# Optimization experiments

Hardware: AMD Instinct MI355X
Metric: run time of the kernel (lower is better)

## Reference

```python
import jax, jax.numpy as jnp
import numpy as np

B, T, P, H, D = 2, 2048, 1024, 16, 128
C = H * D  # 2048
ROPE_THETA = 10000.0


def setup_inputs() -> dict:
    key = jax.random.key(0)
    ks = jax.random.split(key, 5)
    x = jax.random.normal(ks[0], (B, T, C), jnp.float32)
    w_qkv = jax.random.normal(ks[1], (C, 3 * C), jnp.float32) * 0.02  # Linear(dim, 3*dim), applied as x @ w
    w_out = jax.random.normal(ks[2], (C, C), jnp.float32) * 0.02
    past_k = jax.random.normal(ks[3], (B, H, P, D), jnp.float32)
    past_v = jax.random.normal(ks[4], (B, H, P, D), jnp.float32)
    return {"x": x, "w_qkv": w_qkv, "w_out": w_out, "past_k": past_k, "past_v": past_v}


def _rope(q, k, offset):
    # rotate-half RoPE (GPT-NeoX style), positions offset..offset+T-1
    d = q.shape[-1]
    inv_freq = 1.0 / (ROPE_THETA ** (jnp.arange(0, d, 2, dtype=jnp.float32) / d))  # [d/2]
    pos = offset + jnp.arange(q.shape[2], dtype=jnp.float32)                        # [T]
    ang = pos[:, None] * inv_freq[None, :]                                          # [T, d/2]
    cos = jnp.concatenate([jnp.cos(ang), jnp.cos(ang)], -1)[None, None]             # [1,1,T,d]
    sin = jnp.concatenate([jnp.sin(ang), jnp.sin(ang)], -1)[None, None]

    def rot_half(t):
        t1, t2 = jnp.split(t, 2, axis=-1)
        return jnp.concatenate([-t2, t1], -1)

    return q * cos + rot_half(q) * sin, k * cos + rot_half(k) * sin


def reference(x, w_qkv, w_out, past_k, past_v):
    Bv, Tv, Cv = x.shape
    Hn = past_k.shape[1]
    Dd = Cv // Hn
    # fused QKV projection
    qkv = x @ w_qkv                       # [B,T,3C]
    q, k, v = jnp.split(qkv, 3, axis=-1)  # each [B,T,C]

    def split_heads(t):
        return t.reshape(Bv, Tv, Hn, Dd).transpose(0, 2, 1, 3)  # [B,H,T,D]

    q, k, v = split_heads(q), split_heads(k), split_heads(v)
    # RoPE with offset = past length
    q, k = _rope(q, k, past_k.shape[2])
    # KV-cache concat along time axis
    k = jnp.concatenate([past_k, k], axis=2)  # [B,H,P+T,D]
    v = jnp.concatenate([past_v, v], axis=2)
    # SDPA: past_kv present -> is_causal=False, no mask (full attention)
    scale = 1.0 / jnp.sqrt(jnp.float32(Dd))
    scores = jnp.einsum('bhqd,bhkd->bhqk', q, k) * scale
    attn = jax.nn.softmax(scores, axis=-1)
    out = jnp.einsum('bhqk,bhkd->bhqd', attn, v)
    out = out.transpose(0, 2, 1, 3).reshape(Bv, Tv, Cv)
    return out @ w_out
```

## Files before the change

### kernel.cpp

```cpp
#include <hip/hip_runtime.h>
#include <stdint.h>

#define B_ 2
#define T_ 2048
#define P_ 1024
#define H_ 16
#define D_ 128
#define C_ 2048
#define S_ 3072
#define M_ 4096
#define N3_ 6144

typedef unsigned short u16;
typedef unsigned int uint32;
typedef __attribute__((ext_vector_type(8))) short short8;
typedef __attribute__((ext_vector_type(8))) __bf16 bf16x8;
typedef __attribute__((ext_vector_type(4))) float f32x4;
typedef __attribute__((ext_vector_type(16))) float f32x16;
typedef __attribute__((ext_vector_type(4))) unsigned short u16x4;
typedef __attribute__((ext_vector_type(4))) unsigned int uint4v;

static __device__ __forceinline__ float bf2f(u16 h) {
    union { unsigned int u; float f; } x; x.u = ((unsigned int)h) << 16; return x.f;
}
static __device__ __forceinline__ u16 f2bf(float f) {
    return __builtin_bit_cast(u16, (__bf16)f);
}
static __device__ __forceinline__ uint32 cvtpk(float lo, float hi) {
    uint32 r;
    asm("v_cvt_pk_bf16_f32 %0, %1, %2" : "=v"(r) : "v"(lo), "v"(hi));
    return r;
}
#define MAX3(a, b, c) fmaxf(fmaxf((a), (b)), (c))

static __device__ __forceinline__ f32x16 mfma32(short8 a, short8 b, f32x16 c) {
    return __builtin_amdgcn_mfma_f32_32x32x16_bf16(
        __builtin_bit_cast(bf16x8, a), __builtin_bit_cast(bf16x8, b), c, 0, 0, 0);
}

typedef __attribute__((address_space(3))) unsigned int lds_u32;
typedef const __attribute__((address_space(1))) unsigned int glb_u32;
static __device__ __forceinline__ void gload_lds16(const void* g, void* l) {
    __builtin_amdgcn_global_load_lds((glb_u32*)g, (lds_u32*)l, 16, 0, 0);
}

static __device__ __forceinline__ void storeC(float* p, float v) { *p = v; }
static __device__ __forceinline__ void storeC(u16* p, float v) { *p = f2bf(v); }


__global__ void castx_kernel(const float* __restrict__ x, u16* __restrict__ Xb) {
    int idx = blockIdx.x * 256 + threadIdx.x;
    const float4 v = ((const float4*)x)[idx];
    u16x4 o;
    o.x = f2bf(v.x); o.y = f2bf(v.y); o.z = f2bf(v.z); o.w = f2bf(v.w);
    ((u16x4*)Xb)[idx] = o;
}

__global__ void wT_kernel(const float* __restrict__ W, u16* __restrict__ Wt,
                          int Ndim, int Kdim) {
    __shared__ float tile[64][65];
    const int n0 = blockIdx.x * 64, k0 = blockIdx.y * 64;
    const int tid = threadIdx.x;
#pragma unroll
    for (int i = 0; i < 16; i++) {
        int idx = tid + i * 256;
        int r = idx >> 6, c = idx & 63;
        tile[r][c] = W[(size_t)(k0 + r) * Ndim + n0 + c];
    }
    __syncthreads();
#pragma unroll
    for (int i = 0; i < 16; i++) {
        int idx = tid + i * 256;
        int r = idx >> 6, c = idx & 63;
        Wt[(size_t)(n0 + r) * Kdim + k0 + c] = f2bf(tile[c][r]);
    }
}

__global__ void rope_table_kernel(float* __restrict__ cosT, float* __restrict__ sinT) {
    int idx = blockIdx.x * 256 + threadIdx.x;
    int t = idx >> 6, d = idx & 63;
    float inv = powf(10000.0f, -(float)d * (1.0f / 64.0f));
    float ang = (float)(P_ + t) * inv;
    cosT[idx] = cosf(ang);
    sinT[idx] = sinf(ang);
}

__global__ void rope_qk_kernel(u16* __restrict__ QKVb, u16* __restrict__ Kc,
                               const float* __restrict__ cosT,
                               const float* __restrict__ sinT) {
    int idx = blockIdx.x * 256 + threadIdx.x;
    int d = idx & 63;
    int h = (idx >> 6) & 15;
    int t = (idx >> 10) & 2047;
    int b = idx >> 21;
    size_t rowoff = (size_t)(b * T_ + t) * N3_;
    float c = cosT[(t << 6) + d], s = sinT[(t << 6) + d];
    {
        u16* p1 = QKVb + rowoff + h * 128 + d;
        float x1 = bf2f(p1[0]), x2 = bf2f(p1[64]);
        p1[0]  = f2bf(x1 * c - x2 * s);
        p1[64] = f2bf(x2 * c + x1 * s);
    }
    {
        const u16* p1 = QKVb + rowoff + C_ + h * 128 + d;
        float x1 = bf2f(p1[0]), x2 = bf2f(p1[64]);
        u16* o = Kc + ((size_t)(b * H_ + h) * S_ + P_ + t) * 128 + d;
        o[0]  = f2bf(x1 * c - x2 * s);
        o[64] = f2bf(x2 * c + x1 * s);
    }
}

__global__ void pastk_kernel(const float* __restrict__ past_k, u16* __restrict__ Kc) {
    int idx = blockIdx.x * 256 + threadIdx.x;
    int d = idx & 127;
    int p = (idx >> 7) & 1023;
    int bh = idx >> 17;
    Kc[((size_t)bh * S_ + p) * 128 + d] = f2bf(past_k[idx]);
}

__global__ void vnewT_kernel(const u16* __restrict__ QKVb, u16* __restrict__ Vt) {
    __shared__ u16 tile[64][65];
    const int t0 = blockIdx.x * 64, d0 = blockIdx.y * 64, bh = blockIdx.z;
    const int b = bh >> 4, h = bh & 15;
    const int tid = threadIdx.x;
#pragma unroll
    for (int i = 0; i < 16; i++) {
        int idx = tid + i * 256;
        int r = idx >> 6, c = idx & 63;
        tile[r][c] = QKVb[(size_t)(b * T_ + t0 + r) * N3_ + 2 * C_ + h * 128 + d0 + c];
    }
    __syncthreads();
#pragma unroll
    for (int i = 0; i < 16; i++) {
        int idx = tid + i * 256;
        int r = idx >> 6, c = idx & 63;
        Vt[((size_t)bh * 128 + d0 + r) * S_ + P_ + t0 + c] = tile[c][r];
    }
}

__global__ void vpastT_kernel(const float* __restrict__ past_v, u16* __restrict__ Vt) {
    __shared__ float tile[64][65];
    const int p0 = blockIdx.x * 64, d0 = blockIdx.y * 64, bh = blockIdx.z;
    const int tid = threadIdx.x;
#pragma unroll
    for (int i = 0; i < 16; i++) {
        int idx = tid + i * 256;
        int r = idx >> 6, c = idx & 63;
        tile[r][c] = past_v[((size_t)bh * P_ + p0 + r) * 128 + d0 + c];
    }
    __syncthreads();
#pragma unroll
    for (int i = 0; i < 16; i++) {
        int idx = tid + i * 256;
        int r = idx >> 6, c = idx & 63;
        Vt[((size_t)bh * 128 + d0 + r) * S_ + p0 + c] = f2bf(tile[c][r]);
    }
}

template <typename OutT>
__global__ void __launch_bounds__(512, 1)
gemm3(const u16* __restrict__ A, const u16* __restrict__ Bt,
      OutT* __restrict__ Co, int Mdim, int Ndim, int Kdim) {
    __shared__ u16 lA[3 * 256 * 64];
    __shared__ u16 lB[3 * 128 * 64];
    const int nbx = Ndim >> 7;
    const int nwg = (Mdim >> 8) * nbx;
    int bid = blockIdx.x;
    int wg = (bid & 7) * (nwg >> 3) + (bid >> 3);
    const int bm = wg / nbx, bn = wg % nbx;
    const int m0 = bm << 8, n0 = bn << 7;
    const int tid = threadIdx.x;
    const int wave = tid >> 6, lane = tid & 63;
    const int mw = wave >> 1, nw = wave & 1;
    const int l31 = lane & 31, hi = lane >> 5;

    f32x16 acc[2][2];
#pragma unroll
    for (int i = 0; i < 2; i++)
#pragma unroll
        for (int j = 0; j < 2; j++) acc[i][j] = (f32x16)(0.0f);

    const u16* aSrc[4];
    const u16* bSrc[2];
#pragma unroll
    for (int i = 0; i < 4; i++) {
        int cid = i * 512 + tid;
        int r = cid >> 3, pc = cid & 7;
        aSrc[i] = A + (size_t)(m0 + r) * Kdim + ((pc ^ (r & 7)) << 3);
    }
#pragma unroll
    for (int i = 0; i < 2; i++) {
        int cid = i * 512 + tid;
        int r = cid >> 3, pc = cid & 7;
        bSrc[i] = Bt + (size_t)(n0 + r) * Kdim + ((pc ^ (r & 7)) << 3);
    }

#define STAGE3(bi, kt) do {                                                     \
    u16* _pa = lA + (bi) * 16384 + wave * 512;                                  \
    u16* _pb = lB + (bi) * 8192 + wave * 512;                                   \
    _Pragma("unroll")                                                           \
    for (int i = 0; i < 4; i++)                                                 \
        gload_lds16(aSrc[i] + (size_t)(kt) * 64, _pa + i * 4096);               \
    _Pragma("unroll")                                                           \
    for (int i = 0; i < 2; i++)                                                 \
        gload_lds16(bSrc[i] + (size_t)(kt) * 64, _pb + i * 4096);               \
} while (0)

    STAGE3(0, 0);
    STAGE3(1, 1);

    const int NT = Kdim >> 6;
    int bc = 0;
    for (int t = 0; t < NT; ++t) {
        if (t + 1 < NT) asm volatile("s_waitcnt vmcnt(6)" ::: "memory");
        else            asm volatile("s_waitcnt vmcnt(0)" ::: "memory");
        __builtin_amdgcn_s_barrier();
        asm volatile("" ::: "memory");
        if (t + 2 < NT) {
            int b2 = bc + 2; if (b2 >= 3) b2 -= 3;
            STAGE3(b2, t + 2);
        }
        const u16* la = lA + bc * 16384;
        const u16* lb = lB + bc * 8192;
        short8 af[2][4], bf[2][4];
#pragma unroll
        for (int mi = 0; mi < 2; mi++)
#pragma unroll
            for (int ks = 0; ks < 4; ks++) {
                int r = mw * 64 + mi * 32 + l31;
                int cb = ((ks << 5) + (hi << 4)) ^ ((r & 7) << 4);
                af[mi][ks] = *(const short8*)&la[r * 64 + (cb >> 1)];
            }
#pragma unroll
        for (int nj = 0; nj < 2; nj++)
#pragma unroll
            for (int ks = 0; ks < 4; ks++) {
                int r = nw * 64 + nj * 32 + l31;
                int cb = ((ks << 5) + (hi << 4)) ^ ((r & 7) << 4);
                bf[nj][ks] = *(const short8*)&lb[r * 64 + (cb >> 1)];
            }
        __builtin_amdgcn_s_setprio(1);
#pragma unroll
        for (int ks = 0; ks < 4; ks++)
#pragma unroll
            for (int mi = 0; mi < 2; mi++)
#pragma unroll
                for (int nj = 0; nj < 2; nj++)
                    acc[mi][nj] = mfma32(af[mi][ks], bf[nj][ks], acc[mi][nj]);
        __builtin_amdgcn_s_setprio(0);
        __builtin_amdgcn_sched_barrier(0);
        bc = bc + 1; if (bc >= 3) bc = 0;
    }
#undef STAGE3

#pragma unroll
    for (int mi = 0; mi < 2; mi++)
#pragma unroll
        for (int nj = 0; nj < 2; nj++) {
            int col = n0 + nw * 64 + nj * 32 + l31;
#pragma unroll
            for (int g = 0; g < 4; g++) {
                int row = m0 + mw * 64 + mi * 32 + g * 8 + hi * 4;
#pragma unroll
                for (int q = 0; q < 4; q++)
                    storeC(&Co[(size_t)(row + q) * Ndim + col],
                           acc[mi][nj][g * 4 + q]);
            }
        }
}

__global__ void __launch_bounds__(256, 2)
attn_kernel(const u16* __restrict__ QKVb, const u16* __restrict__ Kc,
            const u16* __restrict__ Vt, u16* __restrict__ O) {
    __shared__ u16 ldsK[2][64 * 128];
    __shared__ u16 ldsV[2][128 * 64];

    int bid = blockIdx.x;
    int wg = (bid & 7) * 64 + (bid >> 3);
    const int qc = wg & 15;
    const int bh = wg >> 4;
    const int b = bh >> 4, h = bh & 15;
    const int tid = threadIdx.x, wave = tid >> 6, lane = tid & 63;
    const int l31 = lane & 31, hi = lane >> 5;

    const int krow = tid >> 4;
    const int kcol = (((tid & 15) << 4) ^ ((krow & 7) << 4)) >> 1;
    const int vrow = tid >> 3;
    const int vcol = (((tid & 7) << 4) ^ ((vrow & 7) << 4)) >> 1;

    const u16* Kbh = Kc + (size_t)bh * S_ * 128;
    const u16* Vbh = Vt + (size_t)bh * 128 * S_;

    const int tq = qc * 128 + wave * 32 + l31;
    short8 qf[8];
    {
        const u16* qp = QKVb + (size_t)(b * T_ + tq) * N3_ + h * 128 + hi * 8;
#pragma unroll
        for (int ks = 0; ks < 8; ks++) qf[ks] = *(const short8*)(qp + ks * 16);
    }

    f32x16 acco[4];
#pragma unroll
    for (int d = 0; d < 4; d++) acco[d] = (f32x16)(0.0f);
    float mrow = -1e30f, lrow = 0.f;
    const float sl2 = 0.08838834764831845f * 1.4426950408889634f;

#define STAGE(bufi, tt) do {                                                    \
    const int _s0 = (tt) * 64;                                                  \
    _Pragma("unroll")                                                           \
    for (int i = 0; i < 4; i++)                                                 \
        gload_lds16(Kbh + (size_t)(_s0 + krow + i * 16) * 128 + kcol,           \
                    (char*)&ldsK[bufi][0] + i * 4096 + wave * 1024);            \
    _Pragma("unroll")                                                           \
    for (int i = 0; i < 4; i++)                                                 \
        gload_lds16(Vbh + (size_t)(vrow + i * 32) * S_ + _s0 + vcol,            \
                    (char*)&ldsV[bufi][0] + i * 4096 + wave * 1024);            \
} while (0)

    STAGE(0, 0);
    __syncthreads();

    const int swz = (l31 & 7) << 4;

    for (int t = 0; t < S_ / 64; ++t) {
        const int cur = t & 1;
        if (t < S_ / 64 - 1) STAGE(cur ^ 1, t + 1);

        const u16* Kl = ldsK[cur];
        const u16* Vl = ldsV[cur];

        f32x16 p0 = (f32x16)(0.0f), p1 = (f32x16)(0.0f);
        __builtin_amdgcn_s_setprio(1);
#pragma unroll
        for (int ks = 0; ks < 8; ks++) {
            const int cidx = (((ks * 32 + hi * 16) ^ swz) >> 1);
            short8 k0 = *(const short8*)&Kl[(l31 << 7) + cidx];
            short8 k1 = *(const short8*)&Kl[((32 + l31) << 7) + cidx];
            p0 = mfma32(k0, qf[ks], p0);
            p1 = mfma32(k1, qf[ks], p1);
        }
        __builtin_amdgcn_s_setprio(0);

        float t0 = MAX3(p0[0], p0[1], p0[2]);
        float t1 = MAX3(p0[3], p0[4], p0[5]);
        float t2 = MAX3(p0[6], p0[7], p0[8]);
        float t3 = MAX3(p0[9], p0[10], p0[11]);
        float t4 = MAX3(p0[12], p0[13], p0[14]);
        float t5 = MAX3(p0[15], p1[0], p1[1]);
        float t6 = MAX3(p1[2], p1[3], p1[4]);
        float t7 = MAX3(p1[5], p1[6], p1[7]);
        float t8 = MAX3(p1[8], p1[9], p1[10]);
        float t9 = MAX3(p1[11], p1[12], p1[13]);
        float u0 = MAX3(t0, t1, t2);
        float u1 = MAX3(t3, t4, t5);
        float u2 = MAX3(t6, t7, t8);
        float u3 = MAX3(t9, p1[14], p1[15]);
        float pm = fmaxf(MAX3(u0, u1, u2), u3);
        pm = fmaxf(pm, __shfl_xor(pm, 32));
        float pmS = pm * sl2;
        if (!__all(pmS <= mrow + 8.0f)) {
            float mn = fmaxf(mrow, pmS);
            float fac = exp2f(mrow - mn);
            mrow = mn;
            lrow *= fac;
#pragma unroll
            for (int d = 0; d < 4; d++)
#pragma unroll
                for (int r = 0; r < 16; r++) acco[d][r] *= fac;
        }
        float s0 = 0.f, s1 = 0.f, s2 = 0.f, s3 = 0.f;
#pragma unroll
        for (int r = 0; r < 16; r += 4) {
            p0[r + 0] = exp2f(fmaf(p0[r + 0], sl2, -mrow)); s0 += p0[r + 0];
            p0[r + 1] = exp2f(fmaf(p0[r + 1], sl2, -mrow)); s1 += p0[r + 1];
            p0[r + 2] = exp2f(fmaf(p0[r + 2], sl2, -mrow)); s2 += p0[r + 2];
            p0[r + 3] = exp2f(fmaf(p0[r + 3], sl2, -mrow)); s3 += p0[r + 3];
        }
#pragma unroll
        for (int r = 0; r < 16; r += 4) {
            p1[r + 0] = exp2f(fmaf(p1[r + 0], sl2, -mrow)); s0 += p1[r + 0];
            p1[r + 1] = exp2f(fmaf(p1[r + 1], sl2, -mrow)); s1 += p1[r + 1];
            p1[r + 2] = exp2f(fmaf(p1[r + 2], sl2, -mrow)); s2 += p1[r + 2];
            p1[r + 3] = exp2f(fmaf(p1[r + 3], sl2, -mrow)); s3 += p1[r + 3];
        }
        float sum = (s0 + s1) + (s2 + s3);
        sum += __shfl_xor(sum, 32);
        lrow += sum;

        uint32 w[4][4];
#define PACK_HALF(pp, kh, ksout) do {                                           \
    uint32 A0 = cvtpk(pp[(kh)*8 + 0], pp[(kh)*8 + 1]);                          \
    uint32 A1 = cvtpk(pp[(kh)*8 + 2], pp[(kh)*8 + 3]);                          \
    uint32 B0 = cvtpk(pp[(kh)*8 + 4], pp[(kh)*8 + 5]);                          \
    uint32 B1 = cvtpk(pp[(kh)*8 + 6], pp[(kh)*8 + 7]);                          \
    uint32 sA0 = __shfl_xor(A0, 32), sA1 = __shfl_xor(A1, 32);                  \
    uint32 sB0 = __shfl_xor(B0, 32), sB1 = __shfl_xor(B1, 32);                  \
    w[ksout][0] = hi ? sB0 : A0;                                                \
    w[ksout][1] = hi ? sB1 : A1;                                                \
    w[ksout][2] = hi ? B0 : sA0;                                                \
    w[ksout][3] = hi ? B1 : sA1;                                                \
} while (0)
        PACK_HALF(p0, 0, 0);
        PACK_HALF(p0, 1, 1);
        PACK_HALF(p1, 0, 2);
        PACK_HALF(p1, 1, 3);
#undef PACK_HALF

        __builtin_amdgcn_s_setprio(1);
#pragma unroll
        for (int ks = 0; ks < 4; ks++) {
            uint4v pw = {w[ks][0], w[ks][1], w[ks][2], w[ks][3]};
            short8 pf = __builtin_bit_cast(short8, pw);
            const int cidx = (((ks * 32 + hi * 16) ^ swz) >> 1);
#pragma unroll
            for (int dblk = 0; dblk < 4; dblk++) {
                short8 vf = *(const short8*)&Vl[((dblk * 32 + l31) << 6) + cidx];
                acco[dblk] = mfma32(vf, pf, acco[dblk]);
            }
        }
        __builtin_amdgcn_s_setprio(0);

        __syncthreads();
    }
#undef STAGE

    float rl = 1.0f / lrow;
    u16* Op = O + (size_t)(b * T_ + tq) * C_ + h * 128;
#pragma unroll
    for (int dblk = 0; dblk < 4; dblk++)
#pragma unroll
        for (int j = 0; j < 4; j++) {
            u16x4 o;
            o.x = f2bf(acco[dblk][4 * j + 0] * rl);
            o.y = f2bf(acco[dblk][4 * j + 1] * rl);
            o.z = f2bf(acco[dblk][4 * j + 2] * rl);
            o.w = f2bf(acco[dblk][4 * j + 3] * rl);
            *(u16x4*)(Op + dblk * 32 + j * 8 + hi * 4) = o;
        }
}


extern "C" void kernel_launch(void* const* d_in, const int* in_sizes, int n_in,
                              void* d_out, int out_size, void* d_ws, size_t ws_size,
                              hipStream_t stream) {
    const float* x      = (const float*)d_in[0];
    const float* w_qkv  = (const float*)d_in[1];
    const float* w_out  = (const float*)d_in[2];
    const float* past_k = (const float*)d_in[3];
    const float* past_v = (const float*)d_in[4];
    float* out = (float*)d_out;

    char* ws = (char*)d_ws;
    u16* Xb    = (u16*)(ws);
    u16* Wqkvt = (u16*)(ws + 16777216);
    u16* Woutt = (u16*)(ws + 41943040);
    u16* QKVb  = (u16*)(ws + 50331648);
    u16* Kc    = (u16*)(ws + 100663296);
    u16* Vt    = (u16*)(ws + 125829120);
    u16* O     = (u16*)(ws + 150994944);
    float* cosT = (float*)(ws + 167772160);
    float* sinT = (float*)(ws + 168296448);

    castx_kernel<<<(M_ * C_ / 4) / 256, 256, 0, stream>>>(x, Xb);
    wT_kernel<<<dim3(N3_ / 64, C_ / 64), 256, 0, stream>>>(w_qkv, Wqkvt, N3_, C_);
    wT_kernel<<<dim3(C_ / 64, C_ / 64), 256, 0, stream>>>(w_out, Woutt, C_, C_);
    rope_table_kernel<<<(T_ * 64) / 256, 256, 0, stream>>>(cosT, sinT);

    gemm3<u16><<<(M_ / 256) * (N3_ / 128), 512, 0, stream>>>(Xb, Wqkvt, QKVb, M_, N3_, C_);

    rope_qk_kernel<<<(B_ * T_ * H_ * 64) / 256, 256, 0, stream>>>(QKVb, Kc, cosT, sinT);
    pastk_kernel<<<(B_ * H_ * P_ * D_) / 256, 256, 0, stream>>>(past_k, Kc);
    vnewT_kernel<<<dim3(T_ / 64, 2, B_ * H_), 256, 0, stream>>>(QKVb, Vt);
    vpastT_kernel<<<dim3(P_ / 64, 2, B_ * H_), 256, 0, stream>>>(past_v, Vt);

    attn_kernel<<<512, 256, 0, stream>>>(QKVb, Kc, Vt, O);

    gemm3<float><<<(M_ / 256) * (C_ / 128), 512, 0, stream>>>(O, Woutt, out, M_, C_, C_);
}
```

Baseline: 395.1 us.

## Load V fragments directly from global into registers, bypassing LDS staging

Result: slower. 489.7 us (+23.9%).

```diff
diff --git a/kernel.cpp b/kernel.cpp
--- a/kernel.cpp
+++ b/kernel.cpp
@@ -273,7 +273,6 @@
 attn_kernel(const u16* __restrict__ QKVb, const u16* __restrict__ Kc,
             const u16* __restrict__ Vt, u16* __restrict__ O) {
     __shared__ u16 ldsK[2][64 * 128];
-    __shared__ u16 ldsV[2][128 * 64];
 
     int bid = blockIdx.x;
     int wg = (bid & 7) * 64 + (bid >> 3);
@@ -285,11 +284,10 @@
 
     const int krow = tid >> 4;
     const int kcol = (((tid & 15) << 4) ^ ((krow & 7) << 4)) >> 1;
-    const int vrow = tid >> 3;
-    const int vcol = (((tid & 7) << 4) ^ ((vrow & 7) << 4)) >> 1;
 
     const u16* Kbh = Kc + (size_t)bh * S_ * 128;
     const u16* Vbh = Vt + (size_t)bh * 128 * S_;
+    const u16* Vln = Vbh + (size_t)l31 * S_ + hi * 8;
 
     const int tq = qc * 128 + wave * 32 + l31;
     short8 qf[8];
@@ -305,29 +303,35 @@
     float mrow = -1e30f, lrow = 0.f;
     const float sl2 = 0.08838834764831845f * 1.4426950408889634f;
 
-#define STAGE(bufi, tt) do {                                                    \
+#define STAGEK(bufi, tt) do {                                                   \
     const int _s0 = (tt) * 64;                                                  \
     _Pragma("unroll")                                                           \
     for (int i = 0; i < 4; i++)                                                 \
         gload_lds16(Kbh + (size_t)(_s0 + krow + i * 16) * 128 + kcol,           \
                     (char*)&ldsK[bufi][0] + i * 4096 + wave * 1024);            \
-    _Pragma("unroll")                                                           \
-    for (int i = 0; i < 4; i++)                                                 \
-        gload_lds16(Vbh + (size_t)(vrow + i * 32) * S_ + _s0 + vcol,            \
-                    (char*)&ldsV[bufi][0] + i * 4096 + wave * 1024);            \
 } while (0)
 
-    STAGE(0, 0);
+    STAGEK(0, 0);
     __syncthreads();
 
     const int swz = (l31 & 7) << 4;
 
     for (int t = 0; t < S_ / 64; ++t) {
         const int cur = t & 1;
-        if (t < S_ / 64 - 1) STAGE(cur ^ 1, t + 1);
+        const int s0 = t * 64;
+
+        short8 vf[4][4];
+#pragma unroll
+        for (int ks = 0; ks < 4; ks++)
+#pragma unroll
+            for (int dblk = 0; dblk < 4; dblk++)
+                vf[ks][dblk] = *(const short8*)(Vln + (size_t)(dblk * 32) * S_
+                                                + s0 + ks * 16);
+        __builtin_amdgcn_sched_barrier(0);
+
+        if (t < S_ / 64 - 1) STAGEK(cur ^ 1, t + 1);
 
         const u16* Kl = ldsK[cur];
-        const u16* Vl = ldsV[cur];
 
         f32x16 p0 = (f32x16)(0.0f), p1 = (f32x16)(0.0f);
         __builtin_amdgcn_s_setprio(1);
@@ -368,22 +372,22 @@
 #pragma unroll
                 for (int r = 0; r < 16; r++) acco[d][r] *= fac;
         }
-        float s0 = 0.f, s1 = 0.f, s2 = 0.f, s3 = 0.f;
+        float s0a = 0.f, s1a = 0.f, s2a = 0.f, s3a = 0.f;
 #pragma unroll
         for (int r = 0; r < 16; r += 4) {
-            p0[r + 0] = exp2f(fmaf(p0[r + 0], sl2, -mrow)); s0 += p0[r + 0];
-            p0[r + 1] = exp2f(fmaf(p0[r + 1], sl2, -mrow)); s1 += p0[r + 1];
-            p0[r + 2] = exp2f(fmaf(p0[r + 2], sl2, -mrow)); s2 += p0[r + 2];
-            p0[r + 3] = exp2f(fmaf(p0[r + 3], sl2, -mrow)); s3 += p0[r + 3];
+            p0[r + 0] = exp2f(fmaf(p0[r + 0], sl2, -mrow)); s0a += p0[r + 0];
+            p0[r + 1] = exp2f(fmaf(p0[r + 1], sl2, -mrow)); s1a += p0[r + 1];
+            p0[r + 2] = exp2f(fmaf(p0[r + 2], sl2, -mrow)); s2a += p0[r + 2];
+            p0[r + 3] = exp2f(fmaf(p0[r + 3], sl2, -mrow)); s3a += p0[r + 3];
         }
 #pragma unroll
         for (int r = 0; r < 16; r += 4) {
-            p1[r + 0] = exp2f(fmaf(p1[r + 0], sl2, -mrow)); s0 += p1[r + 0];
-            p1[r + 1] = exp2f(fmaf(p1[r + 1], sl2, -mrow)); s1 += p1[r + 1];
-            p1[r + 2] = exp2f(fmaf(p1[r + 2], sl2, -mrow)); s2 += p1[r + 2];
-            p1[r + 3] = exp2f(fmaf(p1[r + 3], sl2, -mrow)); s3 += p1[r + 3];
-        }
-        float sum = (s0 + s1) + (s2 + s3);
+            p1[r + 0] = exp2f(fmaf(p1[r + 0], sl2, -mrow)); s0a += p1[r + 0];
+            p1[r + 1] = exp2f(fmaf(p1[r + 1], sl2, -mrow)); s1a += p1[r + 1];
+            p1[r + 2] = exp2f(fmaf(p1[r + 2], sl2, -mrow)); s2a += p1[r + 2];
+            p1[r + 3] = exp2f(fmaf(p1[r + 3], sl2, -mrow)); s3a += p1[r + 3];
+        }
+        float sum = (s0a + s1a) + (s2a + s3a);
         sum += __shfl_xor(sum, 32);
         lrow += sum;
 
@@ -411,18 +415,15 @@
         for (int ks = 0; ks < 4; ks++) {
             uint4v pw = {w[ks][0], w[ks][1], w[ks][2], w[ks][3]};
             short8 pf = __builtin_bit_cast(short8, pw);
-            const int cidx = (((ks * 32 + hi * 16) ^ swz) >> 1);
-#pragma unroll
-            for (int dblk = 0; dblk < 4; dblk++) {
-                short8 vf = *(const short8*)&Vl[((dblk * 32 + l31) << 6) + cidx];
-                acco[dblk] = mfma32(vf, pf, acco[dblk]);
-            }
+#pragma unroll
+            for (int dblk = 0; dblk < 4; dblk++)
+                acco[dblk] = mfma32(vf[ks][dblk], pf, acco[dblk]);
         }
         __builtin_amdgcn_s_setprio(0);
 
         __syncthreads();
     }
-#undef STAGE
+#undef STAGEK
 
     float rl = 1.0f / lrow;
     u16* Op = O + (size_t)(b * T_ + tq) * C_ + h * 128;
```
